# Performance work log

Measured on AMD Instinct MI355X. Metric: run time of the kernel, lower is better.

The kernel has to match this reference:

```python
import jax, jax.numpy as jnp
import numpy as np

N_LAYER = 3
N_HEAD = 12
D_K = 64
D_V = 64
D_MODEL = 768
D_INNER = 4096
LN_EPS = 1e-5
BN_EPS = 1e-5
PAD_ID = 1


def _layernorm(x, g, b):
    m = jnp.mean(x, axis=-1, keepdims=True)
    v = jnp.mean((x - m) ** 2, axis=-1, keepdims=True)
    return g * (x - m) / jnp.sqrt(v + LN_EPS) + b


def _batchnorm(x, g, b):
    # training-mode BatchNorm1d: per-feature batch statistics
    m = jnp.mean(x, axis=0)
    v = jnp.mean((x - m) ** 2, axis=0)
    return g * (x - m) / jnp.sqrt(v + BN_EPS) + b


def setup_inputs() -> dict:
    key = jax.random.key(0)
    ks = jax.random.split(key, 24)
    B, C, S, H = 4, 4, 256, D_MODEL
    inp = {
        'input_ids': jax.random.randint(ks[0], (B, C, S), 0, 50000, dtype=jnp.int64) if jax.config.read('jax_enable_x64') else jax.random.randint(ks[0], (B, C, S), 0, 50000, dtype=jnp.int32),
        'roberta_attn': jax.random.normal(ks[1], (B, C, S, H), dtype=jnp.float32),
        'pooled_output': jax.random.normal(ks[2], (B * C, H), dtype=jnp.float32),
        'commonsense_mask': jax.random.uniform(ks[3], (B, C, S, S), dtype=jnp.float32),
        'dependency_mask': jax.random.uniform(ks[4], (B, C, S, S), dtype=jnp.float32),
        'entity_mask': jax.random.uniform(ks[5], (B, C, S), dtype=jnp.float32),
        'sentiment_mask': jax.random.uniform(ks[6], (B, C, S, S), dtype=jnp.float32),
    }
    s = 0.02
    inp['lin_w'] = s * jax.random.normal(ks[7], (H, N_LAYER * 4), dtype=jnp.float32)
    inp['lin_b'] = jnp.zeros((N_LAYER * 4,), jnp.float32)
    inp['Wq'] = s * jax.random.normal(ks[8], (N_LAYER, H, N_HEAD * D_K), dtype=jnp.float32)
    inp['bq'] = jnp.zeros((N_LAYER, N_HEAD * D_K), jnp.float32)
    inp['Wk'] = s * jax.random.normal(ks[9], (N_LAYER, H, N_HEAD * D_K), dtype=jnp.float32)
    inp['bk'] = jnp.zeros((N_LAYER, N_HEAD * D_K), jnp.float32)
    inp['Wv'] = s * jax.random.normal(ks[10], (N_LAYER, H, N_HEAD * D_V), dtype=jnp.float32)
    inp['bv'] = jnp.zeros((N_LAYER, N_HEAD * D_V), jnp.float32)
    inp['Wo'] = s * jax.random.normal(ks[11], (N_LAYER, N_HEAD * D_V, H), dtype=jnp.float32)
    inp['bo'] = jnp.zeros((N_LAYER, H), jnp.float32)
    inp['ln1_g'] = jnp.ones((N_LAYER, H), jnp.float32)
    inp['ln1_b'] = jnp.zeros((N_LAYER, H), jnp.float32)
    inp['W1'] = s * jax.random.normal(ks[12], (N_LAYER, H, D_INNER), dtype=jnp.float32)
    inp['b1'] = jnp.zeros((N_LAYER, D_INNER), jnp.float32)
    inp['W2'] = s * jax.random.normal(ks[13], (N_LAYER, D_INNER, H), dtype=jnp.float32)
    inp['b2'] = jnp.zeros((N_LAYER, H), jnp.float32)
    inp['ln2_g'] = jnp.ones((N_LAYER, H), jnp.float32)
    inp['ln2_b'] = jnp.zeros((N_LAYER, H), jnp.float32)
    inp['bnt_g'] = jnp.ones((H,), jnp.float32)
    inp['bnt_b'] = jnp.zeros((H,), jnp.float32)
    inp['pool_w'] = s * jax.random.normal(ks[14], (H, H), dtype=jnp.float32)
    inp['pool_b'] = jnp.zeros((H,), jnp.float32)
    inp['bn_g'] = jnp.ones((H,), jnp.float32)
    inp['bn_b'] = jnp.zeros((H,), jnp.float32)
    inp['cls_w'] = s * jax.random.normal(ks[15], (H, 1), dtype=jnp.float32)
    inp['cls_b'] = jnp.zeros((1,), jnp.float32)
    return inp


def reference(input_ids, roberta_attn, pooled_output, commonsense_mask, dependency_mask,
              entity_mask, sentiment_mask, lin_w, lin_b, Wq, bq, Wk, bk, Wv, bv, Wo, bo,
              ln1_g, ln1_b, W1, b1, W2, b2, ln2_g, ln2_b, bnt_g, bnt_b,
              pool_w, pool_b, bn_g, bn_b, cls_w, cls_b):
    B, C, S = input_ids.shape
    H = roberta_attn.shape[-1]
    N = B * C
    x = roberta_attn.reshape(N, S, H)

    # learned softmax fusion weights over the 4 relational masks, per layer
    w = jnp.mean(x, axis=1) @ lin_w + lin_b                       # [N, 3*4]
    w = jax.nn.softmax(w.reshape(N, N_LAYER, 4).transpose(1, 0, 2), axis=-1)  # [3, N, 4]

    ent = jnp.broadcast_to(entity_mask[:, :, None, :], (B, C, S, S))
    masks = jnp.stack([
        commonsense_mask.reshape(N, S, S),
        dependency_mask.reshape(N, S, S),
        ent.reshape(N, S, S),
        sentiment_mask.reshape(N, S, S),
    ], axis=1)                                                     # [N, 4, S, S]
    bias = jnp.einsum('lnm,nmqk->lnqk', w, masks)                  # [3, N, S, S]

    non_pad = (input_ids.reshape(N, S) != PAD_ID).astype(x.dtype)[:, :, None]  # [N, S, 1]

    enc = x
    scale = 1.0 / np.sqrt(D_K).astype(np.float32)
    for l in range(N_LAYER):
        residual = enc
        q = (enc @ Wq[l] + bq[l]).reshape(N, S, N_HEAD, D_K)
        k = (enc @ Wk[l] + bk[l]).reshape(N, S, N_HEAD, D_K)
        v = (enc @ Wv[l] + bv[l]).reshape(N, S, N_HEAD, D_V)
        scores = jnp.einsum('nqhd,nkhd->nhqk', q, k) * scale + bias[l][:, None]  # [N,H,S,S]
        attn = jax.nn.softmax(scores, axis=-1)
        o = jnp.einsum('nhqk,nkhd->nqhd', attn, v).reshape(N, S, N_HEAD * D_V)
        o = o @ Wo[l] + bo[l]
        enc = _layernorm(o + residual, ln1_g[l], ln1_b[l]) * non_pad
        residual = enc
        f = jax.nn.relu(enc @ W1[l] + b1[l]) @ W2[l] + b2[l]
        enc = _layernorm(f + residual, ln2_g[l], ln2_b[l]) * non_pad

    enc = _batchnorm(enc.reshape(N * S, H), bnt_g, bnt_b).reshape(N, S, H)
    seq = x + enc
    pooled = jnp.tanh(seq[:, 0] @ pool_w + pool_b)
    pooled = _batchnorm(pooled, bn_g, bn_b)
    logits = pooled @ cls_w + cls_b                                # [N, 1]
    return logits.reshape(-1, C)
```

## Files before the change

kernel.cpp:

```cpp
#include <hip/hip_runtime.h>
#include <hip/hip_bf16.h>
#include <math.h>

#define NSEQ 16
#define SEQ 256
#define H 768
#define NH 12
#define DKH 64
#define DI 4096
#define MROWS (NSEQ*SEQ)
#define QKVN (3*H)

typedef __bf16 v8bf __attribute__((ext_vector_type(8)));
typedef float  v4f  __attribute__((ext_vector_type(4)));
typedef short  v8s  __attribute__((ext_vector_type(8)));

__device__ inline unsigned short bf16b(float f) {
  __hip_bfloat16 h = __float2bfloat16(f);
  return *reinterpret_cast<unsigned short*>(&h);
}
__device__ inline float b2f(unsigned short b) {
  return __uint_as_float(((unsigned int)b) << 16);
}

__device__ __forceinline__ void gload16(const void* g, void* l) {
  __builtin_amdgcn_global_load_lds((const __attribute__((address_space(1))) void*)g,
                                   (__attribute__((address_space(3))) void*)l, 16, 0, 0);
}

__device__ __forceinline__ void waitvm(int n) {
  switch (n) {
    case 0:  asm volatile("s_waitcnt vmcnt(0)" ::: "memory"); break;
    case 2:  asm volatile("s_waitcnt vmcnt(2)" ::: "memory"); break;
    case 4:  asm volatile("s_waitcnt vmcnt(4)" ::: "memory"); break;
    case 8:  asm volatile("s_waitcnt vmcnt(8)" ::: "memory"); break;
    case 12: asm volatile("s_waitcnt vmcnt(12)" ::: "memory"); break;
    case 16: asm volatile("s_waitcnt vmcnt(16)" ::: "memory"); break;
    default: asm volatile("s_waitcnt vmcnt(0)" ::: "memory"); break;
  }
}

enum { MODE_F32_BIAS=0, MODE_BF16_BIAS=1, MODE_BF16_BIAS_RELU=2, MODE_SCORES=3, MODE_PV=4, MODE_F32_NOBIAS=5 };

template<int BM, int BN, int MODE, int BK, int DEPTH, bool SWZ>
__global__ __launch_bounds__(256) void k_mm(
    const unsigned short* __restrict__ A, int lda, long long saN, long long saH,
    const unsigned short* __restrict__ B, int ldb, long long sbN, long long sbH,
    void* __restrict__ Cout, int ldc, long long scN, long long scH,
    const float* __restrict__ bias, int K, int nhdiv) {
  constexpr int MI = BM/32, NI = BN/32;
  constexpr int CH  = BK/8;
  constexpr int RPC = 512/BK;
  constexpr int SW  = CH - 1;
  constexpr int SSH = (BK == 32) ? 1 : 0;
  constexpr int AISS = BM*BK/2048, BISS = BN*BK/2048;
  constexpr int LPT = AISS + BISS;
  constexpr int TA = BM*BK, TB = BN*BK;
  __shared__ unsigned short As[DEPTH*TA];
  __shared__ unsigned short Bs[DEPTH*TB];
  int t = threadIdx.x;
  int z = blockIdx.z, n = z / nhdiv, h = z - n*nhdiv;
  int lane = t & 63, wid = t >> 6, wr = wid >> 1, wc = wid & 1;

  int bx = blockIdx.x, by = blockIdx.y;
  if (SWZ) {
    int gx = gridDim.x;
    int nwg = gx * gridDim.y;
    int lin = by*gx + bx;
    int q = nwg >> 3, r = nwg & 7;
    int xcd = lin & 7, idx = lin >> 3;
    int swz = (xcd < r) ? (xcd*(q+1) + idx) : (r*(q+1) + (xcd-r)*q + idx);
    bx = swz % gx; by = swz / gx;
  }

  const unsigned short* Ab = A + (size_t)n*saN + (size_t)h*saH + (size_t)by*BM*lda;
  const unsigned short* Bb = B + (size_t)n*sbN + (size_t)h*sbH + (size_t)bx*BN*ldb;

  const unsigned short* aSrc[AISS]; int aOff[AISS];
#pragma unroll
  for (int r = 0; r < AISS; ++r) {
    int chunk = wid*AISS + r;
    int row = chunk*RPC + lane/CH;
    int col = ((lane % CH) ^ ((row >> SSH) & SW)) * 8;
    aSrc[r] = Ab + (size_t)row*lda + col;
    aOff[r] = chunk*512;
  }
  const unsigned short* bSrc[BISS]; int bOff[BISS];
#pragma unroll
  for (int r = 0; r < BISS; ++r) {
    int chunk = wid*BISS + r;
    int row = chunk*RPC + lane/CH;
    int col = ((lane % CH) ^ ((row >> SSH) & SW)) * 8;
    bSrc[r] = Bb + (size_t)row*ldb + col;
    bOff[r] = chunk*512;
  }

  v4f acc[MI][NI];
#pragma unroll
  for (int i = 0; i < MI; ++i)
#pragma unroll
    for (int j = 0; j < NI; ++j) acc[i][j] = (v4f){0.f,0.f,0.f,0.f};

  auto issue = [&](int tt, int buf) {
    int k0 = tt * BK;
#pragma unroll
    for (int r = 0; r < AISS; ++r) gload16(aSrc[r] + k0, &As[buf*TA + aOff[r]]);
#pragma unroll
    for (int r = 0; r < BISS; ++r) gload16(bSrc[r] + k0, &Bs[buf*TB + bOff[r]]);
  };

  int nt = K / BK;
  for (int p = 0; p < DEPTH-1 && p < nt; ++p) issue(p, p);
  int cbuf = 0;
  int ibuf = (DEPTH-1) % DEPTH;
  for (int tt = 0; tt < nt; ++tt) {
    int ahead = tt + DEPTH - 1;
    if (ahead < nt) {
      issue(ahead, ibuf);
      waitvm((DEPTH-1)*LPT);
    } else {
      waitvm((nt-1-tt)*LPT);
    }
    __builtin_amdgcn_s_barrier();
    asm volatile("" ::: "memory");
#pragma unroll
    for (int ks = 0; ks < BK/32; ++ks) {
      v8bf af[MI], bfr[NI];
#pragma unroll
      for (int i = 0; i < MI; ++i) {
        int row = wr*(BM/2) + i*16 + (lane & 15);
        int c = (ks*4 + (lane >> 4)) ^ ((row >> SSH) & SW);
        af[i] = *(const v8bf*)&As[cbuf*TA + row*BK + c*8];
      }
#pragma unroll
      for (int j = 0; j < NI; ++j) {
        int row = wc*(BN/2) + j*16 + (lane & 15);
        int c = (ks*4 + (lane >> 4)) ^ ((row >> SSH) & SW);
        bfr[j] = *(const v8bf*)&Bs[cbuf*TB + row*BK + c*8];
      }
#pragma unroll
      for (int i = 0; i < MI; ++i)
#pragma unroll
        for (int j = 0; j < NI; ++j)
          acc[i][j] = __builtin_amdgcn_mfma_f32_16x16x32_bf16(af[i], bfr[j], acc[i][j], 0, 0, 0);
    }
    asm volatile("s_waitcnt lgkmcnt(0)" ::: "memory");
    __builtin_amdgcn_s_barrier();
    asm volatile("" ::: "memory");
    cbuf = (cbuf + 1 == DEPTH) ? 0 : cbuf + 1;
    ibuf = (ibuf + 1 == DEPTH) ? 0 : ibuf + 1;
  }

  float* Cf = (float*)Cout;
  unsigned short* Ch = (unsigned short*)Cout;
  size_t cb = (size_t)n*scN + (size_t)h*scH;
  int grow0 = by*BM + wr*(BM/2);
  int gcol0 = bx*BN + wc*(BN/2);
#pragma unroll
  for (int i = 0; i < MI; ++i) {
#pragma unroll
    for (int j = 0; j < NI; ++j) {
      int col = gcol0 + j*16 + (lane & 15);
      float bval = 0.f;
      if (MODE == MODE_F32_BIAS || MODE == MODE_BF16_BIAS || MODE == MODE_BF16_BIAS_RELU)
        bval = bias[col];
#pragma unroll
      for (int r = 0; r < 4; ++r) {
        int row = grow0 + i*16 + (lane>>4)*4 + r;
        float v = acc[i][j][r];
        if (MODE == MODE_F32_BIAS) {
          Cf[cb + (size_t)row*ldc + col] = v + bval;
        } else if (MODE == MODE_F32_NOBIAS) {
          Cf[cb + (size_t)row*ldc + col] = v;
        } else if (MODE == MODE_PV) {
          Ch[cb + (size_t)row*ldc + col] = bf16b(v);
        } else {
          v += bval;
          if (MODE == MODE_BF16_BIAS_RELU) v = fmaxf(v, 0.f);
          Ch[cb + (size_t)row*ldc + col] = bf16b(v);
        }
      }
    }
  }
}

template<int MODE>
__global__ __launch_bounds__(512) void k_mm256(
    const unsigned short* __restrict__ A, int lda,
    const unsigned short* __restrict__ B, int ldb,
    void* __restrict__ Cout, int ldc,
    const float* __restrict__ bias, int K) {
  extern __shared__ __align__(16) unsigned short smem[];
  unsigned short* As = smem;
  unsigned short* Bs = smem + 2*16384;
  constexpr int TA = 256*64;
  int t = threadIdx.x, lane = t & 63, wid = t >> 6;
  int wr = wid >> 2, wc = wid & 3;

  int bx = blockIdx.x, by = blockIdx.y;
  {
    int gx = gridDim.x, nwg = gx * gridDim.y;
    int lin = by*gx + bx;
    int q = nwg >> 3, r = nwg & 7;
    int xcd = lin & 7, idx = lin >> 3;
    int swz = (xcd < r) ? (xcd*(q+1) + idx) : (r*(q+1) + (xcd-r)*q + idx);
    bx = swz % gx; by = swz / gx;
  }

  const unsigned short* Ab = A + (size_t)by*256*lda;
  const unsigned short* Bb = B + (size_t)bx*256*ldb;

  const unsigned short* aSrc[4]; int aOff[4];
  const unsigned short* bSrc[4]; int bOff[4];
#pragma unroll
  for (int r = 0; r < 4; ++r) {
    int chunk = wid*4 + r;
    int row = chunk*8 + (lane >> 3);
    int col = ((lane & 7) ^ (row & 7)) * 8;
    aSrc[r] = Ab + (size_t)row*lda + col;
    bSrc[r] = Bb + (size_t)row*ldb + col;
    aOff[r] = chunk*512;
    bOff[r] = chunk*512;
  }

  v4f acc[8][4];
#pragma unroll
  for (int i = 0; i < 8; ++i)
#pragma unroll
    for (int j = 0; j < 4; ++j) acc[i][j] = (v4f){0.f,0.f,0.f,0.f};

  auto issue = [&](int tt, int buf) {
    int k0 = tt << 6;
#pragma unroll
    for (int r = 0; r < 4; ++r) gload16(aSrc[r] + k0, &As[buf*TA + aOff[r]]);
#pragma unroll
    for (int r = 0; r < 4; ++r) gload16(bSrc[r] + k0, &Bs[buf*TA + bOff[r]]);
  };

  int nt = K >> 6;
  issue(0, 0);
  int cur = 0;
  for (int tt = 0; tt < nt; ++tt) {
    if (tt + 1 < nt) {
      issue(tt+1, cur^1);
      waitvm(8);
    } else {
      waitvm(0);
    }
    __builtin_amdgcn_s_barrier();
    asm volatile("" ::: "memory");
    __builtin_amdgcn_s_setprio(1);
#pragma unroll
    for (int ks = 0; ks < 2; ++ks) {
      v8bf af[8], bfr[4];
#pragma unroll
      for (int i = 0; i < 8; ++i) {
        int row = wr*128 + i*16 + (lane & 15);
        int c = (ks*4 + (lane >> 4)) ^ (row & 7);
        af[i] = *(const v8bf*)&As[cur*TA + row*64 + c*8];
      }
#pragma unroll
      for (int j = 0; j < 4; ++j) {
        int row = wc*64 + j*16 + (lane & 15);
        int c = (ks*4 + (lane >> 4)) ^ (row & 7);
        bfr[j] = *(const v8bf*)&Bs[cur*TA + row*64 + c*8];
      }
#pragma unroll
      for (int i = 0; i < 8; ++i)
#pragma unroll
        for (int j = 0; j < 4; ++j)
          acc[i][j] = __builtin_amdgcn_mfma_f32_16x16x32_bf16(af[i], bfr[j], acc[i][j], 0, 0, 0);
    }
    __builtin_amdgcn_s_setprio(0);
    asm volatile("s_waitcnt lgkmcnt(0)" ::: "memory");
    __builtin_amdgcn_s_barrier();
    asm volatile("" ::: "memory");
    cur ^= 1;
  }

  float* Cf = (float*)Cout;
  unsigned short* Ch = (unsigned short*)Cout;
  int grow0 = by*256 + wr*128;
  int gcol0 = bx*256 + wc*64;
#pragma unroll
  for (int i = 0; i < 8; ++i) {
#pragma unroll
    for (int j = 0; j < 4; ++j) {
      int col = gcol0 + j*16 + (lane & 15);
      float bval = 0.f;
      if (MODE == MODE_F32_BIAS || MODE == MODE_BF16_BIAS || MODE == MODE_BF16_BIAS_RELU)
        bval = bias[col];
#pragma unroll
      for (int r = 0; r < 4; ++r) {
        int row = grow0 + i*16 + (lane>>4)*4 + r;
        float v = acc[i][j][r];
        if (MODE == MODE_F32_BIAS) {
          Cf[(size_t)row*ldc + col] = v + bval;
        } else if (MODE == MODE_F32_NOBIAS) {
          Cf[(size_t)row*ldc + col] = v;
        } else {
          v += bval;
          if (MODE == MODE_BF16_BIAS_RELU) v = fmaxf(v, 0.f);
          Ch[(size_t)row*ldc + col] = bf16b(v);
        }
      }
    }
  }
}

__global__ __launch_bounds__(256) void k_attn(
    const unsigned short* __restrict__ qkv,
    const unsigned short* __restrict__ vT,
    const unsigned short* __restrict__ biasb,
    unsigned short* __restrict__ O) {
  __shared__ unsigned short Qs[64*64];
  __shared__ unsigned short Ks[256*64];
  __shared__ unsigned short Vs[64*256];
  __shared__ unsigned short Ps[64*256];
  int t = threadIdx.x, lane = t & 63, wid = t >> 6;
  int z = blockIdx.y, n = z / NH, h = z - n*NH;
  int m0 = blockIdx.x * 64;
  const unsigned short* Qb = qkv + (size_t)n*SEQ*QKVN + (size_t)h*DKH + (size_t)m0*QKVN;
  const unsigned short* Kb = qkv + (size_t)n*SEQ*QKVN + H + (size_t)h*DKH;
  const unsigned short* Vb = vT + (size_t)z*DKH*SEQ;
#pragma unroll
  for (int r = 0; r < 2; ++r) {
    int chunk = wid*2 + r;
    int row = chunk*8 + (lane >> 3);
    int col = ((lane & 7) ^ (row & 7)) * 8;
    gload16(Qb + (size_t)row*QKVN + col, &Qs[chunk*512]);
  }
#pragma unroll
  for (int r = 0; r < 8; ++r) {
    int chunk = wid*8 + r;
    int row = chunk*8 + (lane >> 3);
    int col = ((lane & 7) ^ (row & 7)) * 8;
    gload16(Kb + (size_t)row*QKVN + col, &Ks[chunk*512]);
  }
#pragma unroll
  for (int r = 0; r < 8; ++r) {
    int chunk = wid*8 + r;
    int row = chunk*2 + (lane >> 5);
    int cc = lane & 31;
    gload16(Vb + (size_t)row*SEQ + (size_t)((cc ^ (row & 7))*8), &Vs[chunk*512]);
  }
  __syncthreads();

  v4f acc[16];
#pragma unroll
  for (int j = 0; j < 16; ++j) acc[j] = (v4f){0.f,0.f,0.f,0.f};
#pragma unroll
  for (int ks = 0; ks < 2; ++ks) {
    int arow = wid*16 + (lane & 15);
    int ac = (ks*4 + (lane >> 4)) ^ (arow & 7);
    v8bf af = *(const v8bf*)&Qs[arow*64 + ac*8];
#pragma unroll
    for (int j = 0; j < 16; ++j) {
      int brow = j*16 + (lane & 15);
      int bc = (ks*4 + (lane >> 4)) ^ (brow & 7);
      v8bf bf = *(const v8bf*)&Ks[brow*64 + bc*8];
      acc[j] = __builtin_amdgcn_mfma_f32_16x16x32_bf16(af, bf, acc[j], 0, 0, 0);
    }
  }

  int col = lane & 15, quad = lane >> 4;
  const unsigned short* bb = biasb + (size_t)n*65536;
  float e[16][4];
  float rm[4] = {-1e30f, -1e30f, -1e30f, -1e30f};
#pragma unroll
  for (int r = 0; r < 4; ++r) {
    int row = m0 + wid*16 + quad*4 + r;
#pragma unroll
    for (int j = 0; j < 16; ++j) {
      float v = acc[j][r]*0.125f + b2f(bb[(size_t)row*256 + j*16 + col]);
      e[j][r] = v;
      rm[r] = fmaxf(rm[r], v);
    }
  }
#pragma unroll
  for (int r = 0; r < 4; ++r)
#pragma unroll
    for (int m = 1; m < 16; m <<= 1) rm[r] = fmaxf(rm[r], __shfl_xor(rm[r], m, 64));
  float rs[4] = {0.f, 0.f, 0.f, 0.f};
#pragma unroll
  for (int r = 0; r < 4; ++r)
#pragma unroll
    for (int j = 0; j < 16; ++j) {
      float ev = __expf(e[j][r] - rm[r]);
      e[j][r] = ev;
      rs[r] += ev;
    }
#pragma unroll
  for (int r = 0; r < 4; ++r) {
#pragma unroll
    for (int m = 1; m < 16; m <<= 1) rs[r] += __shfl_xor(rs[r], m, 64);
    rs[r] = 1.0f/rs[r];
  }

#pragma unroll
  for (int r = 0; r < 4; ++r) {
    int row = wid*16 + quad*4 + r;
#pragma unroll
    for (int j = 0; j < 16; ++j) {
      int cc = j*2 + (col >> 3);
      Ps[row*256 + ((cc ^ (row & 7))*8) + (col & 7)] = bf16b(e[j][r]*rs[r]);
    }
  }
  asm volatile("s_waitcnt lgkmcnt(0)" ::: "memory");
  __builtin_amdgcn_sched_barrier(0);

  v4f po[4];
#pragma unroll
  for (int j = 0; j < 4; ++j) po[j] = (v4f){0.f,0.f,0.f,0.f};
#pragma unroll
  for (int kk = 0; kk < 8; ++kk) {
    int arow = wid*16 + (lane & 15);
    int c = kk*4 + (lane >> 4);
    v8bf af = *(const v8bf*)&Ps[arow*256 + ((c ^ (arow & 7))*8)];
#pragma unroll
    for (int j = 0; j < 4; ++j) {
      int brow = j*16 + (lane & 15);
      v8bf bf = *(const v8bf*)&Vs[brow*256 + ((c ^ (brow & 7))*8)];
      po[j] = __builtin_amdgcn_mfma_f32_16x16x32_bf16(af, bf, po[j], 0, 0, 0);
    }
  }

  unsigned short* Ob = O + ((size_t)n*SEQ + m0)*H + (size_t)h*DKH;
#pragma unroll
  for (int j = 0; j < 4; ++j) {
    int ocol = j*16 + (lane & 15);
#pragma unroll
    for (int r = 0; r < 4; ++r) {
      int orow = wid*16 + quad*4 + r;
      Ob[(size_t)orow*H + ocol] = bf16b(po[j][r]);
    }
  }
}

__global__ __launch_bounds__(256) void k_wT(const float* __restrict__ in,
                                            unsigned short* __restrict__ out,
                                            int Nn, int Kk) {
  int n0 = blockIdx.x*64, k0 = blockIdx.y*64;
  __shared__ float T[64][72];
  int t = threadIdx.x;
  int r = t >> 4, c4 = (t & 15) * 4;
#pragma unroll
  for (int i = 0; i < 4; ++i) {
    float4 v = *(const float4*)(in + (size_t)(k0 + r + i*16)*Nn + n0 + c4);
    T[c4+0][r+i*16] = v.x; T[c4+1][r+i*16] = v.y;
    T[c4+2][r+i*16] = v.z; T[c4+3][r+i*16] = v.w;
  }
  __syncthreads();
  int c = t >> 3, r8 = (t & 7) * 8;
#pragma unroll
  for (int i = 0; i < 2; ++i) {
    int cc = c + i*32;
    v8s o;
#pragma unroll
    for (int j = 0; j < 8; ++j) o[j] = (short)bf16b(T[cc][r8+j]);
    *(v8s*)(out + (size_t)(n0+cc)*Kk + k0 + r8) = o;
  }
}

__global__ void k_bqkv(const float* __restrict__ bq, const float* __restrict__ bk,
                       const float* __restrict__ bv, float* __restrict__ o) {
  int i = blockIdx.x*256 + threadIdx.x;
  if (i >= 3*QKVN) return;
  int l = i / QKVN, j = i - l*QKVN;
  float v = (j < H) ? bq[l*H + j] : (j < 2*H) ? bk[l*H + j - H] : bv[l*H + j - 2*H];
  o[i] = v;
}

__global__ __launch_bounds__(256) void k_cast(const float* __restrict__ x,
                                              float* __restrict__ enc,
                                              unsigned short* __restrict__ enc16) {
  size_t i = ((size_t)blockIdx.x*256 + threadIdx.x)*4;
  float4 v = *(const float4*)(x + i);
  *(float4*)(enc + i) = v;
  ushort4 u = { bf16b(v.x), bf16b(v.y), bf16b(v.z), bf16b(v.w) };
  *(ushort4*)(enc16 + i) = u;
}

__global__ __launch_bounds__(256) void k_vT(const unsigned short* __restrict__ qkv,
                                            unsigned short* __restrict__ vT) {
  int z = blockIdx.x, n = z/NH, h = z - n*NH;
  const unsigned short* src = qkv + (size_t)n*SEQ*QKVN + 2*H + (size_t)h*DKH;
  __shared__ unsigned short tile[64][264];
  int t = threadIdx.x;
  int r0 = t >> 3, d0 = (t & 7) * 8;
#pragma unroll
  for (int i = 0; i < 8; ++i) {
    int r = r0 + i*32;
    v8s vv = *(const v8s*)(src + (size_t)r*QKVN + d0);
#pragma unroll
    for (int j = 0; j < 8; ++j) tile[d0+j][r] = (unsigned short)vv[j];
  }
  __syncthreads();
  int d = t >> 2, rb = (t & 3) * 64;
  unsigned short* dst = vT + (size_t)z*DKH*SEQ + (size_t)d*SEQ + rb;
#pragma unroll
  for (int i = 0; i < 8; ++i)
    *(v8s*)(dst + i*8) = *(const v8s*)&tile[d][rb + i*8];
}

__global__ __launch_bounds__(256) void k_fusion_weights(
    const float* __restrict__ x, const float* __restrict__ lin_w,
    const float* __restrict__ lin_b, float* __restrict__ wsoft) {
  int n = blockIdx.x, t = threadIdx.x;
  __shared__ float xm[H];
  __shared__ float sred[4];
  __shared__ float logits[12];
  if (t < 192) {
    const float4* p = (const float4*)(x + (size_t)n*SEQ*H) + t;
    float4 s = {0.f,0.f,0.f,0.f};
    for (int r = 0; r < SEQ; ++r) {
      float4 v = p[(size_t)r*192];
      s.x += v.x; s.y += v.y; s.z += v.z; s.w += v.w;
    }
    xm[t*4+0] = s.x*(1.0f/SEQ); xm[t*4+1] = s.y*(1.0f/SEQ);
    xm[t*4+2] = s.z*(1.0f/SEQ); xm[t*4+3] = s.w*(1.0f/SEQ);
  }
  __syncthreads();
  float lacc[12];
#pragma unroll
  for (int j = 0; j < 12; ++j) lacc[j] = 0.f;
  for (int hh = t; hh < H; hh += 256) {
    float xv = xm[hh];
#pragma unroll
    for (int j = 0; j < 12; ++j) lacc[j] += xv * lin_w[hh*12 + j];
  }
  for (int j = 0; j < 12; ++j) {
    float v = lacc[j];
#pragma unroll
    for (int m = 1; m < 64; m <<= 1) v += __shfl_xor(v, m, 64);
    if ((t & 63) == 0) sred[t >> 6] = v;
    __syncthreads();
    if (t == 0) logits[j] = sred[0]+sred[1]+sred[2]+sred[3] + lin_b[j];
    __syncthreads();
  }
  if (t < 3) {
    int l = t;
    float mx = -1e30f;
    for (int m = 0; m < 4; ++m) mx = fmaxf(mx, logits[l*4+m]);
    float e[4], s = 0.f;
    for (int m = 0; m < 4; ++m) { e[m] = expf(logits[l*4+m]-mx); s += e[m]; }
    for (int m = 0; m < 4; ++m) wsoft[(l*NSEQ + n)*4 + m] = e[m]/s;
  }
}

__global__ __launch_bounds__(256) void k_bias(
    const float* __restrict__ cm, const float* __restrict__ dm,
    const float* __restrict__ ent, const float* __restrict__ sm,
    const float* __restrict__ wsoft, int l, unsigned short* __restrict__ bias) {
  int g = blockIdx.x*256 + threadIdx.x;
  int n = g >> 14;
  int k4 = g & 63;
  const float* w = wsoft + (l*NSEQ + n)*4;
  float w0 = w[0], w1 = w[1], w2 = w[2], w3 = w[3];
  float4 c = ((const float4*)cm)[g];
  float4 d = ((const float4*)dm)[g];
  float4 s = ((const float4*)sm)[g];
  float4 e = ((const float4*)(ent + (size_t)n*SEQ))[k4];
  ushort4 o;
  o.x = bf16b(w0*c.x + w1*d.x + w2*e.x + w3*s.x);
  o.y = bf16b(w0*c.y + w1*d.y + w2*e.y + w3*s.y);
  o.z = bf16b(w0*c.z + w1*d.z + w2*e.z + w3*s.z);
  o.w = bf16b(w0*c.w + w1*d.w + w2*e.w + w3*s.w);
  ((ushort4*)bias)[g] = o;
}

__global__ void k_nonpad(const int* __restrict__ ids, float* __restrict__ npad) {
  int i = blockIdx.x*256 + threadIdx.x;
  if (i < MROWS) npad[i] = (ids[i] != 1) ? 1.0f : 0.0f;
}

__global__ __launch_bounds__(256) void k_ln(
    const float* __restrict__ f, float* __restrict__ enc,
    unsigned short* __restrict__ enc16,
    const float* __restrict__ g, const float* __restrict__ b,
    const float* __restrict__ npad) {
  int r = blockIdx.x, t = threadIdx.x;
  size_t base = (size_t)r*H;
  float v0 = f[base+t]     + enc[base+t];
  float v1 = f[base+t+256] + enc[base+t+256];
  float v2 = f[base+t+512] + enc[base+t+512];
  __shared__ float sred[4];
  float s = v0+v1+v2;
#pragma unroll
  for (int m = 1; m < 64; m <<= 1) s += __shfl_xor(s, m, 64);
  if ((t & 63) == 0) sred[t >> 6] = s;
  __syncthreads();
  float mean = (sred[0]+sred[1]+sred[2]+sred[3]) * (1.0f/H);
  __syncthreads();
  float d0 = v0-mean, d1 = v1-mean, d2 = v2-mean;
  float ss = d0*d0 + d1*d1 + d2*d2;
#pragma unroll
  for (int m = 1; m < 64; m <<= 1) ss += __shfl_xor(ss, m, 64);
  if ((t & 63) == 0) sred[t >> 6] = ss;
  __syncthreads();
  float var = (sred[0]+sred[1]+sred[2]+sred[3]) * (1.0f/H);
  float rstd = 1.0f/sqrtf(var + 1e-5f);
  float npv = npad[r];
  float o0 = (g[t]    *d0*rstd + b[t]    )*npv;
  float o1 = (g[t+256]*d1*rstd + b[t+256])*npv;
  float o2 = (g[t+512]*d2*rstd + b[t+512])*npv;
  enc[base+t]     = o0; enc[base+t+256] = o1; enc[base+t+512] = o2;
  enc16[base+t]     = bf16b(o0);
  enc16[base+t+256] = bf16b(o1);
  enc16[base+t+512] = bf16b(o2);
}

__global__ __launch_bounds__(256) void k_ln4(
    const float* __restrict__ p, float* __restrict__ enc,
    unsigned short* __restrict__ enc16,
    const float* __restrict__ g, const float* __restrict__ b,
    const float* __restrict__ npad, const float* __restrict__ cbias) {
  int r = blockIdx.x, t = threadIdx.x;
  size_t base = (size_t)r*H;
  const size_t PS = (size_t)MROWS*H;
  float v0 = p[base+t]     + p[PS+base+t]     + p[2*PS+base+t]     + p[3*PS+base+t]     + cbias[t]     + enc[base+t];
  float v1 = p[base+t+256] + p[PS+base+t+256] + p[2*PS+base+t+256] + p[3*PS+base+t+256] + cbias[t+256] + enc[base+t+256];
  float v2 = p[base+t+512] + p[PS+base+t+512] + p[2*PS+base+t+512] + p[3*PS+base+t+512] + cbias[t+512] + enc[base+t+512];
  __shared__ float sred[4];
  float s = v0+v1+v2;
#pragma unroll
  for (int m = 1; m < 64; m <<= 1) s += __shfl_xor(s, m, 64);
  if ((t & 63) == 0) sred[t >> 6] = s;
  __syncthreads();
  float mean = (sred[0]+sred[1]+sred[2]+sred[3]) * (1.0f/H);
  __syncthreads();
  float d0 = v0-mean, d1 = v1-mean, d2 = v2-mean;
  float ss = d0*d0 + d1*d1 + d2*d2;
#pragma unroll
  for (int m = 1; m < 64; m <<= 1) ss += __shfl_xor(ss, m, 64);
  if ((t & 63) == 0) sred[t >> 6] = ss;
  __syncthreads();
  float var = (sred[0]+sred[1]+sred[2]+sred[3]) * (1.0f/H);
  float rstd = 1.0f/sqrtf(var + 1e-5f);
  float npv = npad[r];
  float o0 = (g[t]    *d0*rstd + b[t]    )*npv;
  float o1 = (g[t+256]*d1*rstd + b[t+256])*npv;
  float o2 = (g[t+512]*d2*rstd + b[t+512])*npv;
  enc[base+t]     = o0; enc[base+t+256] = o1; enc[base+t+512] = o2;
  enc16[base+t]     = bf16b(o0);
  enc16[base+t+256] = bf16b(o1);
  enc16[base+t+512] = bf16b(o2);
}

__global__ __launch_bounds__(256) void k_colstats(
    const float* __restrict__ enc, float* __restrict__ csum, float* __restrict__ csq) {
  int r0 = blockIdx.x*16, t = threadIdx.x;
  float s0=0,s1=0,s2=0,q0=0,q1=0,q2=0;
  for (int r = 0; r < 16; ++r) {
    const float* row = enc + (size_t)(r0+r)*H;
    float a = row[t], b = row[t+256], c = row[t+512];
    s0 += a; s1 += b; s2 += c;
    q0 += a*a; q1 += b*b; q2 += c*c;
  }
  atomicAdd(&csum[t],     s0); atomicAdd(&csum[t+256], s1); atomicAdd(&csum[t+512], s2);
  atomicAdd(&csq[t],      q0); atomicAdd(&csq[t+256],  q1); atomicAdd(&csq[t+512],  q2);
}

__global__ __launch_bounds__(256) void k_poolprep(
    const float* __restrict__ x, const float* __restrict__ enc,
    const float* __restrict__ csum, const float* __restrict__ csq,
    const float* __restrict__ bnt_g, const float* __restrict__ bnt_b,
    float* __restrict__ ps0) {
  int n = blockIdx.x, t = threadIdx.x;
  for (int hh = t; hh < H; hh += 256) {
    float m = csum[hh] * (1.0f/MROWS);
    float var = csq[hh] * (1.0f/MROWS) - m*m;
    float rstd = 1.0f/sqrtf(var + 1e-5f);
    float e = enc[(size_t)n*SEQ*H + hh];
    ps0[n*H + hh] = x[(size_t)n*SEQ*H + hh] + bnt_g[hh]*(e-m)*rstd + bnt_b[hh];
  }
}

__global__ __launch_bounds__(256) void k_poolmm(
    const float* __restrict__ ps0, const float* __restrict__ pool_w,
    const float* __restrict__ pool_b, float* __restrict__ pooled) {
  int n = blockIdx.y, jb = blockIdx.x*64;
  __shared__ float s0[H];
  __shared__ float part[4][64];
  int t = threadIdx.x;
  for (int hh = t; hh < H; hh += 256) s0[hh] = ps0[n*H + hh];
  __syncthreads();
  int j = t & 63, q = t >> 6;
  float a = 0.f;
  int h0 = q*192;
  for (int hh = h0; hh < h0+192; ++hh)
    a = fmaf(s0[hh], pool_w[(size_t)hh*H + jb + j], a);
  part[q][j] = a;
  __syncthreads();
  if (t < 64) {
    float v = part[0][t]+part[1][t]+part[2][t]+part[3][t] + pool_b[jb+t];
    pooled[n*H + jb + t] = tanhf(v);
  }
}

__global__ __launch_bounds__(256) void k_final(
    const float* __restrict__ pooled, const float* __restrict__ bn_g,
    const float* __restrict__ bn_b, const float* __restrict__ cls_w,
    const float* __restrict__ cls_b, float* __restrict__ out) {
  int t = threadIdx.x;
  float acc[16];
#pragma unroll
  for (int n = 0; n < 16; ++n) acc[n] = 0.f;
  for (int hh = t; hh < H; hh += 256) {
    float p[16]; float m = 0.f;
#pragma unroll
    for (int n = 0; n < 16; ++n) { p[n] = pooled[n*H + hh]; m += p[n]; }
    m *= (1.0f/16.f);
    float var = 0.f;
#pragma unroll
    for (int n = 0; n < 16; ++n) { float d = p[n]-m; var += d*d; }
    var *= (1.0f/16.f);
    float rstd = 1.0f/sqrtf(var + 1e-5f);
    float gw = bn_g[hh]*rstd*cls_w[hh];
    float off = bn_b[hh]*cls_w[hh];
#pragma unroll
    for (int n = 0; n < 16; ++n) acc[n] += (p[n]-m)*gw + off;
  }
  __shared__ float sred[4];
  for (int n = 0; n < 16; ++n) {
    float v = acc[n];
#pragma unroll
    for (int m = 1; m < 64; m <<= 1) v += __shfl_xor(v, m, 64);
    if ((t & 63) == 0) sred[t >> 6] = v;
    __syncthreads();
    if (t == 0) out[n] = sred[0]+sred[1]+sred[2]+sred[3] + cls_b[0];
    __syncthreads();
  }
}

extern "C" void kernel_launch(void* const* d_in, const int* in_sizes, int n_in,
                              void* d_out, int out_size, void* d_ws, size_t ws_size,
                              hipStream_t stream) {
  const int*   input_ids = (const int*)  d_in[0];
  const float* x       = (const float*)d_in[1];
  const float* cm      = (const float*)d_in[3];
  const float* dm      = (const float*)d_in[4];
  const float* ent     = (const float*)d_in[5];
  const float* sm      = (const float*)d_in[6];
  const float* lin_w   = (const float*)d_in[7];
  const float* lin_b   = (const float*)d_in[8];
  const float* Wq      = (const float*)d_in[9];
  const float* bq      = (const float*)d_in[10];
  const float* Wk      = (const float*)d_in[11];
  const float* bk      = (const float*)d_in[12];
  const float* Wv      = (const float*)d_in[13];
  const float* bv      = (const float*)d_in[14];
  const float* Wo      = (const float*)d_in[15];
  const float* bo      = (const float*)d_in[16];
  const float* ln1_g   = (const float*)d_in[17];
  const float* ln1_b   = (const float*)d_in[18];
  const float* W1      = (const float*)d_in[19];
  const float* b1      = (const float*)d_in[20];
  const float* W2      = (const float*)d_in[21];
  const float* b2      = (const float*)d_in[22];
  const float* ln2_g   = (const float*)d_in[23];
  const float* ln2_b   = (const float*)d_in[24];
  const float* bnt_g   = (const float*)d_in[25];
  const float* bnt_b   = (const float*)d_in[26];
  const float* pool_w  = (const float*)d_in[27];
  const float* pool_b  = (const float*)d_in[28];
  const float* bn_g    = (const float*)d_in[29];
  const float* bn_b    = (const float*)d_in[30];
  const float* cls_w   = (const float*)d_in[31];
  const float* cls_b   = (const float*)d_in[32];
  float* out = (float*)d_out;
  (void)ws_size; (void)n_in; (void)in_sizes; (void)out_size;

  char* wsb = (char*)d_ws;
  size_t off = 0;
  auto alloc = [&](size_t bytes) {
    void* p = (void*)(wsb + off);
    off += (bytes + 255) & ~(size_t)255;
    return p;
  };
  float* enc            = (float*)alloc((size_t)MROWS*H*4);
  unsigned short* enc16 = (unsigned short*)alloc((size_t)MROWS*H*2);
  unsigned short* qkv16 = (unsigned short*)alloc((size_t)MROWS*QKVN*2);
  unsigned short* vT    = (unsigned short*)alloc((size_t)192*DKH*SEQ*2);
  unsigned short* ob16  = (unsigned short*)alloc((size_t)MROWS*H*2);
  float* fbuf           = (float*)alloc((size_t)4*MROWS*H*4);
  unsigned short* PH    = (unsigned short*)alloc((size_t)MROWS*DI*2);
  unsigned short* hidden16 = PH;
  unsigned short* biasb = (unsigned short*)alloc((size_t)NSEQ*SEQ*SEQ*2);
  unsigned short* WqkvT = (unsigned short*)alloc((size_t)3*QKVN*H*2);
  unsigned short* WoT   = (unsigned short*)alloc((size_t)3*H*H*2);
  unsigned short* W1T   = (unsigned short*)alloc((size_t)3*DI*H*2);
  unsigned short* W2T   = (unsigned short*)alloc((size_t)3*H*DI*2);
  float* bqkv   = (float*)alloc(3*QKVN*4);
  float* wsoft  = (float*)alloc(3*16*4*4);
  float* npad   = (float*)alloc(MROWS*4);
  float* csum   = (float*)alloc(H*4);
  float* csq    = (float*)alloc(H*4);
  float* ps0    = (float*)alloc(16*H*4);
  float* pooled = (float*)alloc(16*H*4);

  k_cast<<<MROWS*H/1024, 256, 0, stream>>>(x, enc, enc16);
  k_fusion_weights<<<16, 256, 0, stream>>>(x, lin_w, lin_b, wsoft);
  k_nonpad<<<MROWS/256, 256, 0, stream>>>(input_ids, npad);
  k_bqkv<<<27, 256, 0, stream>>>(bq, bk, bv, bqkv);
  for (int l = 0; l < 3; ++l) {
    k_wT<<<dim3(12,12), 256, 0, stream>>>(Wq + (size_t)l*H*H, WqkvT + (size_t)l*QKVN*H,           H, H);
    k_wT<<<dim3(12,12), 256, 0, stream>>>(Wk + (size_t)l*H*H, WqkvT + (size_t)l*QKVN*H + H*H,     H, H);
    k_wT<<<dim3(12,12), 256, 0, stream>>>(Wv + (size_t)l*H*H, WqkvT + (size_t)l*QKVN*H + 2*H*H,   H, H);
    k_wT<<<dim3(12,12), 256, 0, stream>>>(Wo + (size_t)l*H*H, WoT + (size_t)l*H*H,                H, H);
    k_wT<<<dim3(64,12), 256, 0, stream>>>(W1 + (size_t)l*H*DI, W1T + (size_t)l*DI*H,              DI, H);
    k_wT<<<dim3(12,64), 256, 0, stream>>>(W2 + (size_t)l*DI*H, W2T + (size_t)l*H*DI,              H, DI);
  }

  for (int l = 0; l < 3; ++l) {
    k_bias<<<1024, 256, 0, stream>>>(cm, dm, ent, sm, wsoft, l, biasb);
    k_mm<128,128,MODE_BF16_BIAS,32,2,true><<<dim3(18,32,1), 256, 0, stream>>>(
        enc16, H, 0, 0, WqkvT + (size_t)l*QKVN*H, H, 0, 0,
        qkv16, QKVN, 0, 0, bqkv + l*QKVN, H, 1);
    k_vT<<<192, 256, 0, stream>>>(qkv16, vT);
    k_attn<<<dim3(4,192), 256, 0, stream>>>(qkv16, vT, biasb, ob16);
    k_mm<64,64,MODE_F32_BIAS,64,3,true><<<dim3(12,64,1), 256, 0, stream>>>(
        ob16, H, 0, 0, WoT + (size_t)l*H*H, H, 0, 0,
        fbuf, H, 0, 0, bo + l*H, H, 1);
    k_ln<<<MROWS, 256, 0, stream>>>(fbuf, enc, enc16, ln1_g + l*H, ln1_b + l*H, npad);
    k_mm256<MODE_BF16_BIAS_RELU><<<dim3(16,16), 512, 131072, stream>>>(
        enc16, H, W1T + (size_t)l*DI*H, H, hidden16, DI, b1 + l*DI, H);
    k_mm<128,128,MODE_F32_NOBIAS,32,2,true><<<dim3(6,32,4), 256, 0, stream>>>(
        hidden16, DI, 0, 1024, W2T + (size_t)l*H*DI, DI, 0, 1024,
        fbuf, H, 0, (long long)MROWS*H, nullptr, 1024, 4);
    k_ln4<<<MROWS, 256, 0, stream>>>(fbuf, enc, enc16, ln2_g + l*H, ln2_b + l*H, npad, b2 + l*H);
  }

  hipMemsetAsync(csum, 0, H*sizeof(float), stream);
  hipMemsetAsync(csq,  0, H*sizeof(float), stream);
  k_colstats<<<256, 256, 0, stream>>>(enc, csum, csq);
  k_poolprep<<<16, 256, 0, stream>>>(x, enc, csum, csq, bnt_g, bnt_b, ps0);
  k_poolmm<<<dim3(12,16), 256, 0, stream>>>(ps0, pool_w, pool_b, pooled);
  k_final<<<1, 256, 0, stream>>>(pooled, bn_g, bn_b, cls_w, cls_b, out);
}
```

Measured before the change: 643.1 us.

## Fuse V transpose into attention, reuse K smem for P, halve W2 split-K

The attention kernel now reads V directly from the QKV buffer and transposes it into swizzled shared memory itself, which removes the separate k_vT kernel and its global round trip. The probability tile P now reuses the K shared buffer, guarded by an added barrier, so the kernel needs less LDS and can fit more blocks per CU. The W2 GEMM switches from 4-way to 2-way split-K with 128x64 tiles, so there are fewer partial buffers for the following layernorm to sum. The costs are scalar LDS stores during the V transpose, an extra block-wide sync, and longer K loops in the W2 GEMM.

```diff
diff --git a/kernel.cpp b/kernel.cpp
--- a/kernel.cpp
+++ b/kernel.cpp
@@ -310,19 +310,18 @@
 
 __global__ __launch_bounds__(256) void k_attn(
     const unsigned short* __restrict__ qkv,
-    const unsigned short* __restrict__ vT,
     const unsigned short* __restrict__ biasb,
     unsigned short* __restrict__ O) {
   __shared__ unsigned short Qs[64*64];
   __shared__ unsigned short Ks[256*64];
   __shared__ unsigned short Vs[64*256];
-  __shared__ unsigned short Ps[64*256];
+  unsigned short* Ps = Ks;
   int t = threadIdx.x, lane = t & 63, wid = t >> 6;
   int z = blockIdx.y, n = z / NH, h = z - n*NH;
   int m0 = blockIdx.x * 64;
   const unsigned short* Qb = qkv + (size_t)n*SEQ*QKVN + (size_t)h*DKH + (size_t)m0*QKVN;
   const unsigned short* Kb = qkv + (size_t)n*SEQ*QKVN + H + (size_t)h*DKH;
-  const unsigned short* Vb = vT + (size_t)z*DKH*SEQ;
+  const unsigned short* Vb = qkv + (size_t)n*SEQ*QKVN + 2*H + (size_t)h*DKH;
 #pragma unroll
   for (int r = 0; r < 2; ++r) {
     int chunk = wid*2 + r;
@@ -337,12 +336,19 @@
     int col = ((lane & 7) ^ (row & 7)) * 8;
     gload16(Kb + (size_t)row*QKVN + col, &Ks[chunk*512]);
   }
-#pragma unroll
-  for (int r = 0; r < 8; ++r) {
-    int chunk = wid*8 + r;
-    int row = chunk*2 + (lane >> 5);
-    int cc = lane & 31;
-    gload16(Vb + (size_t)row*SEQ + (size_t)((cc ^ (row & 7))*8), &Vs[chunk*512]);
+  {
+    int kr0 = t >> 3, d0 = (t & 7) * 8;
+#pragma unroll
+    for (int i = 0; i < 8; ++i) {
+      int k = kr0 + i*32;
+      v8s vv = *(const v8s*)(Vb + (size_t)k*QKVN + d0);
+      int kc = k >> 3, ke = k & 7;
+#pragma unroll
+      for (int j = 0; j < 8; ++j) {
+        int d = d0 + j;
+        Vs[d*256 + ((kc ^ (d & 7)) << 3) + ke] = (unsigned short)vv[j];
+      }
+    }
   }
   __syncthreads();
 
@@ -396,6 +402,8 @@
     for (int m = 1; m < 16; m <<= 1) rs[r] += __shfl_xor(rs[r], m, 64);
     rs[r] = 1.0f/rs[r];
   }
+
+  __syncthreads();
 
 #pragma unroll
   for (int r = 0; r < 4; ++r) {
@@ -479,28 +487,6 @@
   *(float4*)(enc + i) = v;
   ushort4 u = { bf16b(v.x), bf16b(v.y), bf16b(v.z), bf16b(v.w) };
   *(ushort4*)(enc16 + i) = u;
-}
-
-__global__ __launch_bounds__(256) void k_vT(const unsigned short* __restrict__ qkv,
-                                            unsigned short* __restrict__ vT) {
-  int z = blockIdx.x, n = z/NH, h = z - n*NH;
-  const unsigned short* src = qkv + (size_t)n*SEQ*QKVN + 2*H + (size_t)h*DKH;
-  __shared__ unsigned short tile[64][264];
-  int t = threadIdx.x;
-  int r0 = t >> 3, d0 = (t & 7) * 8;
-#pragma unroll
-  for (int i = 0; i < 8; ++i) {
-    int r = r0 + i*32;
-    v8s vv = *(const v8s*)(src + (size_t)r*QKVN + d0);
-#pragma unroll
-    for (int j = 0; j < 8; ++j) tile[d0+j][r] = (unsigned short)vv[j];
-  }
-  __syncthreads();
-  int d = t >> 2, rb = (t & 3) * 64;
-  unsigned short* dst = vT + (size_t)z*DKH*SEQ + (size_t)d*SEQ + rb;
-#pragma unroll
-  for (int i = 0; i < 8; ++i)
-    *(v8s*)(dst + i*8) = *(const v8s*)&tile[d][rb + i*8];
 }
 
 __global__ __launch_bounds__(256) void k_fusion_weights(
@@ -610,7 +596,7 @@
   enc16[base+t+512] = bf16b(o2);
 }
 
-__global__ __launch_bounds__(256) void k_ln4(
+__global__ __launch_bounds__(256) void k_ln2(
     const float* __restrict__ p, float* __restrict__ enc,
     unsigned short* __restrict__ enc16,
     const float* __restrict__ g, const float* __restrict__ b,
@@ -618,9 +604,9 @@
   int r = blockIdx.x, t = threadIdx.x;
   size_t base = (size_t)r*H;
   const size_t PS = (size_t)MROWS*H;
-  float v0 = p[base+t]     + p[PS+base+t]     + p[2*PS+base+t]     + p[3*PS+base+t]     + cbias[t]     + enc[base+t];
-  float v1 = p[base+t+256] + p[PS+base+t+256] + p[2*PS+base+t+256] + p[3*PS+base+t+256] + cbias[t+256] + enc[base+t+256];
-  float v2 = p[base+t+512] + p[PS+base+t+512] + p[2*PS+base+t+512] + p[3*PS+base+t+512] + cbias[t+512] + enc[base+t+512];
+  float v0 = p[base+t]     + p[PS+base+t]     + cbias[t]     + enc[base+t];
+  float v1 = p[base+t+256] + p[PS+base+t+256] + cbias[t+256] + enc[base+t+256];
+  float v2 = p[base+t+512] + p[PS+base+t+512] + cbias[t+512] + enc[base+t+512];
   __shared__ float sred[4];
   float s = v0+v1+v2;
 #pragma unroll
@@ -781,9 +767,8 @@
   float* enc            = (float*)alloc((size_t)MROWS*H*4);
   unsigned short* enc16 = (unsigned short*)alloc((size_t)MROWS*H*2);
   unsigned short* qkv16 = (unsigned short*)alloc((size_t)MROWS*QKVN*2);
-  unsigned short* vT    = (unsigned short*)alloc((size_t)192*DKH*SEQ*2);
   unsigned short* ob16  = (unsigned short*)alloc((size_t)MROWS*H*2);
-  float* fbuf           = (float*)alloc((size_t)4*MROWS*H*4);
+  float* fbuf           = (float*)alloc((size_t)2*MROWS*H*4);
   unsigned short* PH    = (unsigned short*)alloc((size_t)MROWS*DI*2);
   unsigned short* hidden16 = PH;
   unsigned short* biasb = (unsigned short*)alloc((size_t)NSEQ*SEQ*SEQ*2);
@@ -817,18 +802,17 @@
     k_mm<128,128,MODE_BF16_BIAS,32,2,true><<<dim3(18,32,1), 256, 0, stream>>>(
         enc16, H, 0, 0, WqkvT + (size_t)l*QKVN*H, H, 0, 0,
         qkv16, QKVN, 0, 0, bqkv + l*QKVN, H, 1);
-    k_vT<<<192, 256, 0, stream>>>(qkv16, vT);
-    k_attn<<<dim3(4,192), 256, 0, stream>>>(qkv16, vT, biasb, ob16);
+    k_attn<<<dim3(4,192), 256, 0, stream>>>(qkv16, biasb, ob16);
     k_mm<64,64,MODE_F32_BIAS,64,3,true><<<dim3(12,64,1), 256, 0, stream>>>(
         ob16, H, 0, 0, WoT + (size_t)l*H*H, H, 0, 0,
         fbuf, H, 0, 0, bo + l*H, H, 1);
     k_ln<<<MROWS, 256, 0, stream>>>(fbuf, enc, enc16, ln1_g + l*H, ln1_b + l*H, npad);
     k_mm256<MODE_BF16_BIAS_RELU><<<dim3(16,16), 512, 131072, stream>>>(
         enc16, H, W1T + (size_t)l*DI*H, H, hidden16, DI, b1 + l*DI, H);
-    k_mm<128,128,MODE_F32_NOBIAS,32,2,true><<<dim3(6,32,4), 256, 0, stream>>>(
-        hidden16, DI, 0, 1024, W2T + (size_t)l*H*DI, DI, 0, 1024,
-        fbuf, H, 0, (long long)MROWS*H, nullptr, 1024, 4);
-    k_ln4<<<MROWS, 256, 0, stream>>>(fbuf, enc, enc16, ln2_g + l*H, ln2_b + l*H, npad, b2 + l*H);
+    k_mm<128,64,MODE_F32_NOBIAS,32,2,true><<<dim3(12,32,2), 256, 0, stream>>>(
+        hidden16, DI, 0, 2048, W2T + (size_t)l*H*DI, DI, 0, 2048,
+        fbuf, H, 0, (long long)MROWS*H, nullptr, 2048, 2);
+    k_ln2<<<MROWS, 256, 0, stream>>>(fbuf, enc, enc16, ln2_g + l*H, ln2_b + l*H, npad, b2 + l*H);
   }
 
   hipMemsetAsync(csum, 0, H*sizeof(float), stream);
```

New measurement: 638.1 us. No clear change (-0.8%).
